# Kernel tuning notes

Measured on AMD Instinct MI355X. Metric: run time of the kernel, lower is better.

The kernel has to match this reference:

```python
import jax, jax.numpy as jnp
import numpy as np

B, T, D, H = 16, 512, 512, 8
TE = 2048
DH = D // H


def _ln(x, g, b, eps=1e-5):
    m = jnp.mean(x, axis=-1, keepdims=True)
    v = jnp.mean((x - m) ** 2, axis=-1, keepdims=True)
    return (x - m) * jax.lax.rsqrt(v + eps) * g + b


def setup_inputs() -> dict:
    key = jax.random.key(0)
    ks = jax.random.split(key, 16)
    s = 0.02
    inp = {
        "x1": jax.random.normal(ks[0], (B, T, D), jnp.float32),
        "x2": jax.random.normal(ks[1], (B, T, D), jnp.float32),
        "emb": jax.random.normal(ks[2], (2 * B, TE), jnp.float32),
        "src_mask": jnp.ones((2 * B, T, T, 1), jnp.float32),
        # LayerNorm params (x-norm and text-norm)
        "ln_x_g": jnp.ones((D,), jnp.float32), "ln_x_b": jnp.zeros((D,), jnp.float32),
        "ln_t_g": jnp.ones((D,), jnp.float32), "ln_t_b": jnp.zeros((D,), jnp.float32),
        # Q/K/V projections, stored as [in, out]
        "Wq": jax.random.normal(ks[3], (D, D), jnp.float32) * s, "bq": jnp.zeros((D,), jnp.float32),
        "Wk": jax.random.normal(ks[4], (D, D), jnp.float32) * s, "bk": jnp.zeros((D,), jnp.float32),
        "Wv": jax.random.normal(ks[5], (D, D), jnp.float32) * s, "bv": jnp.zeros((D,), jnp.float32),
        # StylizationBlock: SiLU->Linear(TE, 2D), LayerNorm(D), SiLU->Linear(D, D)
        "Wemb": jax.random.normal(ks[6], (TE, 2 * D), jnp.float32) * s, "bemb": jnp.zeros((2 * D,), jnp.float32),
        "sb_g": jnp.ones((D,), jnp.float32), "sb_b": jnp.zeros((D,), jnp.float32),
        "Wout": jax.random.normal(ks[7], (D, D), jnp.float32) * s, "bout": jnp.zeros((D,), jnp.float32),
    }
    return inp


def reference(x1, x2, emb, src_mask,
              ln_x_g, ln_x_b, ln_t_g, ln_t_b,
              Wq, bq, Wk, bk, Wv, bv,
              Wemb, bemb, sb_g, sb_b, Wout, bout):
    # cross=True: swap-concat the two interacting streams
    xa = jnp.concatenate([x1, x2], axis=0)  # [2B,T,D] (query side)
    xb = jnp.concatenate([x2, x1], axis=0)  # [2B,T,D] (key/value side)
    B2 = xa.shape[0]

    xn = _ln(xa, ln_x_g, ln_x_b)
    tn = _ln(xb, ln_t_g, ln_t_b)

    q = (xn @ Wq + bq).reshape(B2, T, H, DH)
    k = (tn @ Wk + bk).reshape(B2, T, H, DH)
    v = (tn @ Wv + bv).reshape(B2, T, H, DH)

    attn = jnp.einsum('bnhd,bmhd->bnmh', q, k) / np.sqrt(DH).astype(np.float32)
    attn = attn + (1.0 - src_mask) * -100000.0
    w = jax.nn.softmax(attn, axis=2)  # softmax over key axis m

    y = jnp.einsum('bnmh,bmhd->bnhd', w, v).reshape(B2, T, D)

    # StylizationBlock: FiLM from emb, then SiLU + Linear
    emb_out = (jax.nn.silu(emb) @ Wemb + bemb)[:, None, :]  # [2B,1,2D]
    scale, shift = jnp.split(emb_out, 2, axis=2)
    h = _ln(y, sb_g, sb_b) * (1.0 + scale) + shift
    h = jax.nn.silu(h) @ Wout + bout

    out = xa + h
    return out[:B2 // 2], out[B2 // 2:]
```

## Files before the change

### kernel.cpp

```cpp
#include <hip/hip_runtime.h>
#include <hip/hip_bf16.h>
#include <stdint.h>


typedef float f32x4 __attribute__((ext_vector_type(4)));
typedef short s16x8 __attribute__((ext_vector_type(8)));

#define MFMA16(a, b, c) __builtin_amdgcn_mfma_f32_16x16x32_bf16((a), (b), (c), 0, 0, 0)
#define GLD16(g, l) __builtin_amdgcn_global_load_lds( \
    (const __attribute__((address_space(1))) void*)(g), \
    (__attribute__((address_space(3))) void*)(l), 16, 0, 0)

__device__ __forceinline__ ushort f2bf(float f) {
    union { float f; uint32_t u; } cv; cv.f = f;
    uint32_t u = cv.u;
    return (ushort)((u + 0x7fffu + ((u >> 16) & 1u)) >> 16);
}
__device__ __forceinline__ float bf2f(ushort u) {
    union { uint32_t u; float f; } cv; cv.u = ((uint32_t)u) << 16;
    return cv.f;
}
__device__ __forceinline__ uint32_t pack_bf2(float a, float b) {
    union { float f; uint32_t u; } x, y; x.f = a; y.f = b;
    return ((x.u + 0x8000u) >> 16) | ((y.u + 0x8000u) & 0xffff0000u);
}
__device__ __forceinline__ float fast_exp2(float x) {
#if __has_builtin(__builtin_amdgcn_exp2f)
    return __builtin_amdgcn_exp2f(x);
#else
    return exp2f(x);
#endif
}
__device__ __forceinline__ float wave_sum(float v) {
#pragma unroll
    for (int o = 32; o > 0; o >>= 1) v += __shfl_xor(v, o);
    return v;
}

#define QSCALE 0.180336880f
#define MNEG  -144269.504f

__global__ __launch_bounds__(256) void prep(
    const float* __restrict__ w0, const float* __restrict__ w1,
    const float* __restrict__ w2, const float* __restrict__ w3,
    ushort* __restrict__ o0, ushort* __restrict__ o1,
    ushort* __restrict__ o2, ushort* __restrict__ o3,
    const float* __restrict__ x1, const float* __restrict__ x2,
    const float* __restrict__ gx, const float* __restrict__ bx,
    const float* __restrict__ gt, const float* __restrict__ bt,
    ushort* __restrict__ xn, ushort* __restrict__ tn,
    const float* __restrict__ mask, int* __restrict__ flags,
    const float* __restrict__ bemb, float* __restrict__ ss) {
    __shared__ float tile[32][33];
    __shared__ int bad4[4];
    const int bid = blockIdx.x, tid = threadIdx.x;

    if (bid < 1024) {
        const int z = bid >> 8, xy = bid & 255;
        const float* src; ushort* dst;
        switch (z) {
            case 0: src = w0; dst = o0; break;
            case 1: src = w1; dst = o1; break;
            case 2: src = w2; dst = o2; break;
            default: src = w3; dst = o3; break;
        }
        const int n0 = (xy & 15) * 32, k0 = (xy >> 4) * 32;
        const int x = tid & 31, y0 = tid >> 5;
#pragma unroll
        for (int i = 0; i < 4; i++) {
            int yy = y0 + 8 * i;
            tile[yy][x] = src[(size_t)(k0 + yy) * 512 + n0 + x];
        }
        __syncthreads();
#pragma unroll
        for (int i = 0; i < 4; i++) {
            int yy = y0 + 8 * i;
            dst[(size_t)(n0 + yy) * 512 + k0 + x] = f2bf(tile[x][yy]);
        }
    } else if (bid < 5120) {
        const int r = (bid - 1024) * 4 + (tid >> 6);
        const int lane = tid & 63;
        const float* src = (r < 8192) ? x1 + (size_t)r * 512
                                      : x2 + (size_t)(r - 8192) * 512;
        const int tr = (r < 8192) ? r + 8192 : r - 8192;
        const int d0 = lane * 4;
        float4 a0 = *(const float4*)&src[d0];
        float4 a1 = *(const float4*)&src[d0 + 256];
        float s = a0.x + a0.y + a0.z + a0.w + a1.x + a1.y + a1.z + a1.w;
        float q = a0.x*a0.x + a0.y*a0.y + a0.z*a0.z + a0.w*a0.w
                + a1.x*a1.x + a1.y*a1.y + a1.z*a1.z + a1.w*a1.w;
        s = wave_sum(s); q = wave_sum(q);
        const float mean = s * (1.f/512.f);
        const float var = q * (1.f/512.f) - mean * mean;
        const float rs = rsqrtf(var + 1e-5f);
        float vals[8] = {a0.x, a0.y, a0.z, a0.w, a1.x, a1.y, a1.z, a1.w};
        ushort* px = xn + (size_t)r * 512;
        ushort* pt = tn + (size_t)tr * 512;
#pragma unroll
        for (int half = 0; half < 2; half++) {
            ushort4 ox, ot;
            ushort* pox = (ushort*)&ox; ushort* pot = (ushort*)&ot;
#pragma unroll
            for (int j = 0; j < 4; j++) {
                int d = d0 + half * 256 + j;
                float nv = (vals[half * 4 + j] - mean) * rs;
                pox[j] = f2bf(nv * gx[d] + bx[d]);
                pot[j] = f2bf(nv * gt[d] + bt[d]);
            }
            *(ushort4*)&px[d0 + half * 256] = ox;
            *(ushort4*)&pt[d0 + half * 256] = ot;
        }
    } else if (bid < 7168) {
        const int b = bid - 5120;
        const int b2 = b >> 6, qt = (b >> 3) & 7, kt = b & 7;
        const int r = tid >> 2, c4 = tid & 3;
        const float* mrow = mask + ((size_t)(b2 * 512 + qt * 64 + r)) * 512 + kt * 64;
        bool bad = false;
#pragma unroll
        for (int j = 0; j < 4; j++) {
            float4 v = *(const float4*)&mrow[(c4 + 4 * j) * 4];
            bad |= (v.x != 1.f) | (v.y != 1.f) | (v.z != 1.f) | (v.w != 1.f);
        }
        unsigned long long bl = __ballot(bad);
        const int w = tid >> 6;
        if ((tid & 63) == 0) bad4[w] = (bl != 0ull);
        __syncthreads();
        if (tid == 0) flags[b] = bad4[0] | bad4[1] | bad4[2] | bad4[3];
    } else {
        int i = (bid - 7168) * 256 + tid;
        ss[i] = bemb[i & 1023];
    }
}

__global__ __launch_bounds__(256) void emb_gemm(const float* __restrict__ emb,
                                                const float* __restrict__ Wemb,
                                                float* __restrict__ ss) {
    __shared__ float es[32 * 128];
    const int n0 = blockIdx.x * 128, k0 = blockIdx.y * 128;
    const int t = threadIdx.x;
#pragma unroll
    for (int i = 0; i < 16; i++) {
        int idx = t + 256 * i;
        int b = idx >> 7, kk = idx & 127;
        float v = emb[(size_t)b * 2048 + k0 + kk];
        es[idx] = v / (1.f + __expf(-v));
    }
    __syncthreads();
    const int n = n0 + (t & 127);
    const int kh = (t >> 7) * 64;
    float acc[32];
#pragma unroll
    for (int b = 0; b < 32; b++) acc[b] = 0.f;
    for (int kk = kh; kk < kh + 64; kk++) {
        float w = Wemb[(size_t)(k0 + kk) * 1024 + n];
#pragma unroll
        for (int b = 0; b < 32; b++) acc[b] += es[b * 128 + kk] * w;
    }
#pragma unroll
    for (int b = 0; b < 32; b++) atomicAdd(&ss[b * 1024 + n], acc[b]);
}

__global__ __launch_bounds__(256, 3) void gemm_qkv(
    const ushort* __restrict__ xn, const ushort* __restrict__ tn,
    const ushort* __restrict__ W,
    const float* __restrict__ bq, const float* __restrict__ bk,
    const float* __restrict__ bv,
    ushort* __restrict__ qb, ushort* __restrict__ kb,
    ushort* __restrict__ vtb) {
    __shared__ ushort As[128 * 64];
    __shared__ ushort Bs[128 * 64];
    const int tid = threadIdx.x;
    const int lane = tid & 63, w = tid >> 6;
    const int l15 = lane & 15, quad = lane >> 4;
    const int l8 = lane >> 3, c_src = (lane & 7) ^ l8;
    const int bid = blockIdx.x;
    const int xcd = bid & 7, j = bid >> 3;
    const int mt_l = j / 12, nt = j % 12;
    const int m0 = (xcd * 16 + mt_l) * 128, n0 = nt * 128;
    const ushort* A = (n0 < 512) ? xn : tn;
    const int wm = (w >> 1) * 64, wn = (w & 1) * 64;

    f32x4 zero = {0.f, 0.f, 0.f, 0.f};
    f32x4 acc[4][4];
#pragma unroll
    for (int i = 0; i < 4; i++)
#pragma unroll
        for (int jj = 0; jj < 4; jj++) acc[i][jj] = zero;

    const ushort* ga0 = A + (size_t)(m0 + w * 32 + l8) * 512 + c_src * 8;
    const ushort* gb0 = W + (size_t)(n0 + w * 32 + l8) * 512 + c_src * 8;

    for (int k0 = 0; k0 < 512; k0 += 64) {
#pragma unroll
        for (int i = 0; i < 4; i++) {
            GLD16(ga0 + (size_t)(i * 8) * 512 + k0, &As[(w * 32 + i * 8) * 64]);
            GLD16(gb0 + (size_t)(i * 8) * 512 + k0, &Bs[(w * 32 + i * 8) * 64]);
        }
        __syncthreads();
#pragma unroll
        for (int ks = 0; ks < 2; ks++) {
            const int sl = ((ks * 4 + quad) ^ (l15 & 7)) * 8;
            s16x8 af[4], bf[4];
#pragma unroll
            for (int i = 0; i < 4; i++)
                af[i] = *(const s16x8*)&As[(wm + i * 16 + l15) * 64 + sl];
#pragma unroll
            for (int jj = 0; jj < 4; jj++)
                bf[jj] = *(const s16x8*)&Bs[(wn + jj * 16 + l15) * 64 + sl];
#pragma unroll
            for (int i = 0; i < 4; i++)
#pragma unroll
                for (int jj = 0; jj < 4; jj++)
                    acc[i][jj] = MFMA16(af[i], bf[jj], acc[i][jj]);
        }
        __syncthreads();
    }

#pragma unroll
    for (int i = 0; i < 4; i++)
#pragma unroll
        for (int jj = 0; jj < 4; jj++) {
            const int col = n0 + wn + jj * 16 + l15;
            if (n0 < 512) {
                const float bvv = bq[col];
#pragma unroll
                for (int reg = 0; reg < 4; reg++) {
                    const int row = m0 + wm + i * 16 + quad * 4 + reg;
                    qb[(size_t)row * 512 + col] = f2bf((acc[i][jj][reg] + bvv) * QSCALE);
                }
            } else if (n0 < 1024) {
                const int ck = col - 512;
                const float bvv = bk[ck];
#pragma unroll
                for (int reg = 0; reg < 4; reg++) {
                    const int row = m0 + wm + i * 16 + quad * 4 + reg;
                    kb[(size_t)row * 512 + ck] = f2bf(acc[i][jj][reg] + bvv);
                }
            } else {
                const int c2 = col - 1024;
                const float bvv = bv[c2];
                const int b2 = m0 >> 9;
                const int t0 = (m0 & 511) + wm + i * 16 + quad * 4;
                ushort4 o4; ushort* po = (ushort*)&o4;
#pragma unroll
                for (int reg = 0; reg < 4; reg++)
                    po[reg] = f2bf(acc[i][jj][reg] + bvv);
                *(ushort4*)&vtb[((size_t)((b2 * 8 + (c2 >> 6)) * 64 + (c2 & 63))) * 512 + t0] = o4;
            }
        }
}

__global__ __launch_bounds__(256, 3) void gemm_out(
    const ushort* __restrict__ A, const ushort* __restrict__ Bt,
    const float* __restrict__ bias, float* __restrict__ of,
    const float* __restrict__ r1, const float* __restrict__ r2) {
    __shared__ ushort As[128 * 64];
    __shared__ ushort Bs[128 * 64];
    const int tid = threadIdx.x;
    const int lane = tid & 63, w = tid >> 6;
    const int l15 = lane & 15, quad = lane >> 4;
    const int l8 = lane >> 3, c_src = (lane & 7) ^ l8;
    const int bid = blockIdx.x;
    const int xcd = bid & 7, j2 = bid >> 3;
    const int m0 = (xcd * 16 + (j2 >> 2)) * 128;
    const int n0 = (j2 & 3) * 128;
    const int wm = (w >> 1) * 64, wn = (w & 1) * 64;

    f32x4 zero = {0.f, 0.f, 0.f, 0.f};
    f32x4 acc[4][4];
#pragma unroll
    for (int i = 0; i < 4; i++)
#pragma unroll
        for (int jj = 0; jj < 4; jj++) acc[i][jj] = zero;

    const ushort* ga0 = A + (size_t)(m0 + w * 32 + l8) * 512 + c_src * 8;
    const ushort* gb0 = Bt + (size_t)(n0 + w * 32 + l8) * 512 + c_src * 8;

    for (int k0 = 0; k0 < 512; k0 += 64) {
#pragma unroll
        for (int i = 0; i < 4; i++) {
            GLD16(ga0 + (size_t)(i * 8) * 512 + k0, &As[(w * 32 + i * 8) * 64]);
            GLD16(gb0 + (size_t)(i * 8) * 512 + k0, &Bs[(w * 32 + i * 8) * 64]);
        }
        __syncthreads();
#pragma unroll
        for (int ks = 0; ks < 2; ks++) {
            const int sl = ((ks * 4 + quad) ^ (l15 & 7)) * 8;
            s16x8 af[4], bf[4];
#pragma unroll
            for (int i = 0; i < 4; i++)
                af[i] = *(const s16x8*)&As[(wm + i * 16 + l15) * 64 + sl];
#pragma unroll
            for (int jj = 0; jj < 4; jj++)
                bf[jj] = *(const s16x8*)&Bs[(wn + jj * 16 + l15) * 64 + sl];
#pragma unroll
            for (int i = 0; i < 4; i++)
#pragma unroll
                for (int jj = 0; jj < 4; jj++)
                    acc[i][jj] = MFMA16(af[i], bf[jj], acc[i][jj]);
        }
        __syncthreads();
    }

#pragma unroll
    for (int i = 0; i < 4; i++)
#pragma unroll
        for (int jj = 0; jj < 4; jj++) {
            const int col = n0 + wn + jj * 16 + l15;
            const float bvv = bias[col];
#pragma unroll
            for (int reg = 0; reg < 4; reg++) {
                const int row = m0 + wm + i * 16 + quad * 4 + reg;
                float res = (row < 8192)
                                ? r1[(size_t)row * 512 + col]
                                : r2[(size_t)(row - 8192) * 512 + col];
                of[(size_t)row * 512 + col] = acc[i][jj][reg] + bvv + res;
            }
        }
}

__global__ __launch_bounds__(256) void attn(
    const ushort* __restrict__ q, const ushort* __restrict__ k,
    const ushort* __restrict__ vt, const float* __restrict__ mask,
    const int* __restrict__ flags, ushort* __restrict__ y) {
    __shared__ ushort Ks[2][64 * 64];
    __shared__ ushort Vs[2][64 * 64];
    __shared__ ushort Ps[4][16 * 72];
    const int tid = threadIdx.x;
    const int lane = tid & 63, w = tid >> 6;
    const int l15 = lane & 15, quad = lane >> 4;
    const int l8 = lane >> 3, c_src = (lane & 7) ^ l8;
    const int bh = blockIdx.x, qt = blockIdx.y;
    const int b2 = bh >> 3, h = bh & 7;
    const int qrow0 = qt * 64 + w * 16;

    s16x8 qf0, qf1;
    {
        const ushort* qp = q + ((size_t)(b2 * 512 + qrow0 + l15)) * 512 + h * 64 + quad * 8;
        qf0 = *(const s16x8*)qp;
        qf1 = *(const s16x8*)(qp + 32);
    }
    f32x4 zero = {0.f, 0.f, 0.f, 0.f};
    f32x4 o[4];
#pragma unroll
    for (int nt = 0; nt < 4; nt++) o[nt] = zero;
    float l_i = 0.f;

    const ushort* kg0 = k + ((size_t)(b2 * 512 + w * 16 + l8)) * 512 + h * 64 + c_src * 8;
    const ushort* vg0 = vt + ((size_t)(bh * 64 + w * 16 + l8)) * 512 + c_src * 8;
    ushort* Pw = &Ps[w][0];
    const int slq = (quad ^ (l15 & 7)) * 8;
    const int slq4 = ((4 + quad) ^ (l15 & 7)) * 8;
    const int fl_base = (b2 * 8 + qt) * 8;

    auto stage = [&](int buf, int kt) {
        GLD16(kg0 + (size_t)(kt * 64) * 512, &Ks[buf][(w * 16) * 64]);
        GLD16(kg0 + (size_t)(kt * 64 + 8) * 512, &Ks[buf][(w * 16 + 8) * 64]);
        GLD16(vg0 + kt * 64, &Vs[buf][(w * 16) * 64]);
        GLD16(vg0 + (size_t)8 * 512 + kt * 64, &Vs[buf][(w * 16 + 8) * 64]);
    };
    stage(0, 0);

    for (int kt = 0; kt < 8; kt++) {
        __syncthreads();
        if (kt < 7) stage((kt + 1) & 1, kt + 1);
        const ushort* Kb = Ks[kt & 1];
        const ushort* Vb = Vs[kt & 1];

        f32x4 st[4];
#pragma unroll
        for (int mt = 0; mt < 4; mt++) {
            const int row = (mt * 16 + l15) * 64;
            s16x8 kf0 = *(const s16x8*)&Kb[row + slq];
            s16x8 kf1 = *(const s16x8*)&Kb[row + slq4];
            st[mt] = MFMA16(kf0, qf0, zero);
            st[mt] = MFMA16(kf1, qf1, st[mt]);
        }

        if (flags[fl_base + kt]) {
            const size_t mb = ((size_t)(b2 * 512 + qt * 64 + w * 16 + l15)) * 512 + kt * 64;
#pragma unroll
            for (int mt = 0; mt < 4; mt++)
#pragma unroll
                for (int reg = 0; reg < 4; reg++)
                    st[mt][reg] += (1.f - mask[mb + mt * 16 + quad * 4 + reg]) * MNEG;
        }

        float psum = 0.f;
#pragma unroll
        for (int mt = 0; mt < 4; mt++) {
            float p0 = fast_exp2(st[mt][0]);
            float p1 = fast_exp2(st[mt][1]);
            float p2 = fast_exp2(st[mt][2]);
            float p3 = fast_exp2(st[mt][3]);
            psum += (p0 + p1) + (p2 + p3);
            uint2 pk;
            pk.x = pack_bf2(p0, p1);
            pk.y = pack_bf2(p2, p3);
            *(uint2*)&Pw[l15 * 72 + mt * 16 + quad * 4] = pk;
        }

        s16x8 pf0 = *(const s16x8*)&Pw[l15 * 72 + quad * 8];
        s16x8 pf1 = *(const s16x8*)&Pw[l15 * 72 + 32 + quad * 8];
#pragma unroll
        for (int nt = 0; nt < 4; nt++) {
            const int vr = (nt * 16 + l15) * 64;
            s16x8 vf0 = *(const s16x8*)&Vb[vr + slq];
            s16x8 vf1 = *(const s16x8*)&Vb[vr + slq4];
            o[nt] = MFMA16(pf0, vf0, o[nt]);
            o[nt] = MFMA16(pf1, vf1, o[nt]);
        }

        psum += __shfl_xor(psum, 16);
        psum += __shfl_xor(psum, 32);
        l_i += psum;
    }

    const float invl = 1.f / l_i;
    float ir[4];
#pragma unroll
    for (int reg = 0; reg < 4; reg++) ir[reg] = __shfl(invl, quad * 4 + reg);
#pragma unroll
    for (int reg = 0; reg < 4; reg++) {
        const int row = qt * 64 + w * 16 + quad * 4 + reg;
        ushort* yp = y + ((size_t)(b2 * 512 + row)) * 512 + h * 64;
#pragma unroll
        for (int nt = 0; nt < 4; nt++)
            yp[nt * 16 + l15] = f2bf(o[nt][reg] * ir[reg]);
    }
}

__global__ __launch_bounds__(256) void film_silu(
    const ushort* __restrict__ y, const float* __restrict__ g,
    const float* __restrict__ b, const float* __restrict__ ss,
    ushort* __restrict__ tb) {
    const int r = blockIdx.x * 4 + (threadIdx.x >> 6);
    const int lane = threadIdx.x & 63;
    const int b2 = r >> 9;
    const int d0 = lane * 8;
    s16x8 raw = *(const s16x8*)&y[(size_t)r * 512 + d0];
    float v[8];
#pragma unroll
    for (int j = 0; j < 8; j++) v[j] = bf2f((ushort)raw[j]);
    float s = 0.f, qq = 0.f;
#pragma unroll
    for (int j = 0; j < 8; j++) { s += v[j]; qq += v[j] * v[j]; }
    s = wave_sum(s); qq = wave_sum(qq);
    const float mean = s * (1.f/512.f);
    const float var = qq * (1.f/512.f) - mean * mean;
    const float rs = rsqrtf(var + 1e-5f);
    const float* scp = ss + (size_t)b2 * 1024;
    s16x8 o;
#pragma unroll
    for (int j = 0; j < 8; j++) {
        int d = d0 + j;
        float ln = (v[j] - mean) * rs * g[d] + b[d];
        float hv = ln * (1.f + scp[d]) + scp[512 + d];
        o[j] = (short)f2bf(hv / (1.f + __expf(-hv)));
    }
    *(s16x8*)&tb[(size_t)r * 512 + d0] = o;
}

extern "C" void kernel_launch(void* const* d_in, const int* in_sizes, int n_in,
                              void* d_out, int out_size, void* d_ws, size_t ws_size,
                              hipStream_t stream) {
    const float* x1     = (const float*)d_in[0];
    const float* x2     = (const float*)d_in[1];
    const float* emb    = (const float*)d_in[2];
    const float* mask   = (const float*)d_in[3];
    const float* ln_x_g = (const float*)d_in[4];
    const float* ln_x_b = (const float*)d_in[5];
    const float* ln_t_g = (const float*)d_in[6];
    const float* ln_t_b = (const float*)d_in[7];
    const float* Wq     = (const float*)d_in[8];
    const float* bq     = (const float*)d_in[9];
    const float* Wk     = (const float*)d_in[10];
    const float* bk     = (const float*)d_in[11];
    const float* Wv     = (const float*)d_in[12];
    const float* bv     = (const float*)d_in[13];
    const float* Wemb   = (const float*)d_in[14];
    const float* bemb   = (const float*)d_in[15];
    const float* sb_g   = (const float*)d_in[16];
    const float* sb_b   = (const float*)d_in[17];
    const float* Wout   = (const float*)d_in[18];
    const float* bout   = (const float*)d_in[19];
    float* out = (float*)d_out;

    char* ws = (char*)d_ws;
    ushort* xn   = (ushort*)(ws + 0);
    ushort* tn   = (ushort*)(ws + (16u << 20));
    ushort* qb   = (ushort*)(ws + (32u << 20));
    ushort* kb   = (ushort*)(ws + (48u << 20));
    ushort* vtb  = (ushort*)(ws + (64u << 20));
    ushort* yb   = (ushort*)(ws + (80u << 20));
    ushort* wqkv = (ushort*)(ws + (96u << 20));
    ushort* wto  = wqkv + 786432;
    float*  ss   = (float*)(ws + (98u << 20));
    int*    flg  = (int*)(ws + (98u << 20) + (128u << 10));
    ushort* tb   = xn;

    prep<<<7296, 256, 0, stream>>>(Wq, Wk, Wv, Wout,
                                   wqkv, wqkv + 262144, wqkv + 524288, wto,
                                   x1, x2, ln_x_g, ln_x_b, ln_t_g, ln_t_b, xn, tn,
                                   mask, flg, bemb, ss);

    emb_gemm<<<dim3(8, 16), 256, 0, stream>>>(emb, Wemb, ss);

    gemm_qkv<<<1536, 256, 0, stream>>>(xn, tn, wqkv, bq, bk, bv, qb, kb, vtb);

    attn<<<dim3(256, 8), 256, 0, stream>>>(qb, kb, vtb, mask, flg, yb);

    film_silu<<<4096, 256, 0, stream>>>(yb, sb_g, sb_b, ss, tb);

    gemm_out<<<512, 256, 0, stream>>>(tb, wto, bout, out, x1, x2);

    (void)in_sizes; (void)n_in; (void)out_size; (void)ws_size;
}
```

Baseline: 294.3 us.

## Load K/V attention fragments directly from global into registers, dropping LDS staging

The attention kernel no longer stages K and V tiles in shared memory with async global-to-LDS copies and per-tile barriers. Each wave now loads its K and V MFMA fragments straight from global memory into registers and prefetches the next K tile one iteration ahead. It also sets a launch bound of three blocks per CU. This removes the __syncthreads and LDS traffic, but each of the four waves now fetches the same K/V data separately and register pressure rises, which may force spills.

```diff
diff --git a/kernel.cpp b/kernel.cpp
--- a/kernel.cpp
+++ b/kernel.cpp
@@ -319,17 +319,14 @@
         }
 }
 
-__global__ __launch_bounds__(256) void attn(
+__global__ __launch_bounds__(256, 3) void attn(
     const ushort* __restrict__ q, const ushort* __restrict__ k,
     const ushort* __restrict__ vt, const float* __restrict__ mask,
     const int* __restrict__ flags, ushort* __restrict__ y) {
-    __shared__ ushort Ks[2][64 * 64];
-    __shared__ ushort Vs[2][64 * 64];
     __shared__ ushort Ps[4][16 * 72];
     const int tid = threadIdx.x;
     const int lane = tid & 63, w = tid >> 6;
     const int l15 = lane & 15, quad = lane >> 4;
-    const int l8 = lane >> 3, c_src = (lane & 7) ^ l8;
     const int bh = blockIdx.x, qt = blockIdx.y;
     const int b2 = bh >> 3, h = bh & 7;
     const int qrow0 = qt * 64 + w * 16;
@@ -346,35 +343,42 @@
     for (int nt = 0; nt < 4; nt++) o[nt] = zero;
     float l_i = 0.f;
 
-    const ushort* kg0 = k + ((size_t)(b2 * 512 + w * 16 + l8)) * 512 + h * 64 + c_src * 8;
-    const ushort* vg0 = vt + ((size_t)(bh * 64 + w * 16 + l8)) * 512 + c_src * 8;
+    const ushort* kbase = k + ((size_t)(b2 * 512 + l15)) * 512 + h * 64 + quad * 8;
+    const ushort* vbase = vt + ((size_t)(bh * 64 + l15)) * 512 + quad * 8;
     ushort* Pw = &Ps[w][0];
-    const int slq = (quad ^ (l15 & 7)) * 8;
-    const int slq4 = ((4 + quad) ^ (l15 & 7)) * 8;
     const int fl_base = (b2 * 8 + qt) * 8;
 
-    auto stage = [&](int buf, int kt) {
-        GLD16(kg0 + (size_t)(kt * 64) * 512, &Ks[buf][(w * 16) * 64]);
-        GLD16(kg0 + (size_t)(kt * 64 + 8) * 512, &Ks[buf][(w * 16 + 8) * 64]);
-        GLD16(vg0 + kt * 64, &Vs[buf][(w * 16) * 64]);
-        GLD16(vg0 + (size_t)8 * 512 + kt * 64, &Vs[buf][(w * 16 + 8) * 64]);
-    };
-    stage(0, 0);
+    s16x8 kc[8];
+#pragma unroll
+    for (int mt = 0; mt < 4; mt++) {
+        const ushort* p = kbase + (size_t)(mt * 16) * 512;
+        kc[2 * mt] = *(const s16x8*)p;
+        kc[2 * mt + 1] = *(const s16x8*)(p + 32);
+    }
 
     for (int kt = 0; kt < 8; kt++) {
-        __syncthreads();
-        if (kt < 7) stage((kt + 1) & 1, kt + 1);
-        const ushort* Kb = Ks[kt & 1];
-        const ushort* Vb = Vs[kt & 1];
+        s16x8 vf[8];
+#pragma unroll
+        for (int nt = 0; nt < 4; nt++) {
+            const ushort* p = vbase + (size_t)(nt * 16) * 512 + kt * 64;
+            vf[2 * nt] = *(const s16x8*)p;
+            vf[2 * nt + 1] = *(const s16x8*)(p + 32);
+        }
+        s16x8 kn[8];
+        if (kt < 7) {
+#pragma unroll
+            for (int mt = 0; mt < 4; mt++) {
+                const ushort* p = kbase + (size_t)((kt + 1) * 64 + mt * 16) * 512;
+                kn[2 * mt] = *(const s16x8*)p;
+                kn[2 * mt + 1] = *(const s16x8*)(p + 32);
+            }
+        }
 
         f32x4 st[4];
 #pragma unroll
         for (int mt = 0; mt < 4; mt++) {
-            const int row = (mt * 16 + l15) * 64;
-            s16x8 kf0 = *(const s16x8*)&Kb[row + slq];
-            s16x8 kf1 = *(const s16x8*)&Kb[row + slq4];
-            st[mt] = MFMA16(kf0, qf0, zero);
-            st[mt] = MFMA16(kf1, qf1, st[mt]);
+            st[mt] = MFMA16(kc[2 * mt], qf0, zero);
+            st[mt] = MFMA16(kc[2 * mt + 1], qf1, st[mt]);
         }
 
         if (flags[fl_base + kt]) {
@@ -404,16 +408,16 @@
         s16x8 pf1 = *(const s16x8*)&Pw[l15 * 72 + 32 + quad * 8];
 #pragma unroll
         for (int nt = 0; nt < 4; nt++) {
-            const int vr = (nt * 16 + l15) * 64;
-            s16x8 vf0 = *(const s16x8*)&Vb[vr + slq];
-            s16x8 vf1 = *(const s16x8*)&Vb[vr + slq4];
-            o[nt] = MFMA16(pf0, vf0, o[nt]);
-            o[nt] = MFMA16(pf1, vf1, o[nt]);
+            o[nt] = MFMA16(pf0, vf[2 * nt], o[nt]);
+            o[nt] = MFMA16(pf1, vf[2 * nt + 1], o[nt]);
         }
 
         psum += __shfl_xor(psum, 16);
         psum += __shfl_xor(psum, 32);
         l_i += psum;
+
+#pragma unroll
+        for (int i = 0; i < 8; i++) kc[i] = kn[i];
     }
 
     const float invl = 1.f / l_i;
```

After: 373.0 us. 26.7% more time.

## Process 32 query rows per wave in attention to reuse K/V tiles

Applied to the files above, without the earlier changes.

Each attention wave now handles two 16-row query sub-tiles instead of one, so every K and V fragment read from LDS feeds twice as many MFMAs. The grid's query-tile dimension is halved, which halves total K/V global-to-LDS staging. Mask flag indexing is adjusted to the 64-row flag granularity, and launch bounds request 3 blocks per CU. The cost is more registers per thread for the doubled accumulators, a larger P buffer in LDS, and fewer blocks in the grid.

```diff
diff --git a/kernel.cpp b/kernel.cpp
--- a/kernel.cpp
+++ b/kernel.cpp
@@ -319,39 +319,42 @@
         }
 }
 
-__global__ __launch_bounds__(256) void attn(
+__global__ __launch_bounds__(256, 3) void attn(
     const ushort* __restrict__ q, const ushort* __restrict__ k,
     const ushort* __restrict__ vt, const float* __restrict__ mask,
     const int* __restrict__ flags, ushort* __restrict__ y) {
     __shared__ ushort Ks[2][64 * 64];
     __shared__ ushort Vs[2][64 * 64];
-    __shared__ ushort Ps[4][16 * 72];
+    __shared__ ushort Ps[4][32 * 72];
     const int tid = threadIdx.x;
     const int lane = tid & 63, w = tid >> 6;
     const int l15 = lane & 15, quad = lane >> 4;
     const int l8 = lane >> 3, c_src = (lane & 7) ^ l8;
     const int bh = blockIdx.x, qt = blockIdx.y;
     const int b2 = bh >> 3, h = bh & 7;
-    const int qrow0 = qt * 64 + w * 16;
-
-    s16x8 qf0, qf1;
-    {
-        const ushort* qp = q + ((size_t)(b2 * 512 + qrow0 + l15)) * 512 + h * 64 + quad * 8;
-        qf0 = *(const s16x8*)qp;
-        qf1 = *(const s16x8*)(qp + 32);
+    const int qrow0 = qt * 128 + w * 32;
+
+    s16x8 qf[2][2];
+#pragma unroll
+    for (int qi = 0; qi < 2; qi++) {
+        const ushort* qp = q + ((size_t)(b2 * 512 + qrow0 + qi * 16 + l15)) * 512 + h * 64 + quad * 8;
+        qf[qi][0] = *(const s16x8*)qp;
+        qf[qi][1] = *(const s16x8*)(qp + 32);
     }
     f32x4 zero = {0.f, 0.f, 0.f, 0.f};
-    f32x4 o[4];
-#pragma unroll
-    for (int nt = 0; nt < 4; nt++) o[nt] = zero;
-    float l_i = 0.f;
+    f32x4 o[2][4];
+#pragma unroll
+    for (int qi = 0; qi < 2; qi++)
+#pragma unroll
+        for (int nt = 0; nt < 4; nt++) o[qi][nt] = zero;
+    float l_i[2] = {0.f, 0.f};
 
     const ushort* kg0 = k + ((size_t)(b2 * 512 + w * 16 + l8)) * 512 + h * 64 + c_src * 8;
     const ushort* vg0 = vt + ((size_t)(bh * 64 + w * 16 + l8)) * 512 + c_src * 8;
     ushort* Pw = &Ps[w][0];
     const int slq = (quad ^ (l15 & 7)) * 8;
     const int slq4 = ((4 + quad) ^ (l15 & 7)) * 8;
-    const int fl_base = (b2 * 8 + qt) * 8;
+    const int fl_base = (b2 * 8 + qt * 2 + (w >> 1)) * 8;
 
     auto stage = [&](int buf, int kt) {
         GLD16(kg0 + (size_t)(kt * 64) * 512, &Ks[buf][(w * 16) * 64]);
@@ -367,66 +370,82 @@
         const ushort* Kb = Ks[kt & 1];
         const ushort* Vb = Vs[kt & 1];
 
-        f32x4 st[4];
+        f32x4 st[2][4];
 #pragma unroll
         for (int mt = 0; mt < 4; mt++) {
             const int row = (mt * 16 + l15) * 64;
             s16x8 kf0 = *(const s16x8*)&Kb[row + slq];
             s16x8 kf1 = *(const s16x8*)&Kb[row + slq4];
-            st[mt] = MFMA16(kf0, qf0, zero);
-            st[mt] = MFMA16(kf1, qf1, st[mt]);
+            st[0][mt] = MFMA16(kf0, qf[0][0], zero);
+            st[0][mt] = MFMA16(kf1, qf[0][1], st[0][mt]);
+            st[1][mt] = MFMA16(kf0, qf[1][0], zero);
+            st[1][mt] = MFMA16(kf1, qf[1][1], st[1][mt]);
         }
 
         if (flags[fl_base + kt]) {
-            const size_t mb = ((size_t)(b2 * 512 + qt * 64 + w * 16 + l15)) * 512 + kt * 64;
-#pragma unroll
-            for (int mt = 0; mt < 4; mt++)
-#pragma unroll
-                for (int reg = 0; reg < 4; reg++)
-                    st[mt][reg] += (1.f - mask[mb + mt * 16 + quad * 4 + reg]) * MNEG;
-        }
-
-        float psum = 0.f;
-#pragma unroll
-        for (int mt = 0; mt < 4; mt++) {
-            float p0 = fast_exp2(st[mt][0]);
-            float p1 = fast_exp2(st[mt][1]);
-            float p2 = fast_exp2(st[mt][2]);
-            float p3 = fast_exp2(st[mt][3]);
-            psum += (p0 + p1) + (p2 + p3);
-            uint2 pk;
-            pk.x = pack_bf2(p0, p1);
-            pk.y = pack_bf2(p2, p3);
-            *(uint2*)&Pw[l15 * 72 + mt * 16 + quad * 4] = pk;
-        }
-
-        s16x8 pf0 = *(const s16x8*)&Pw[l15 * 72 + quad * 8];
-        s16x8 pf1 = *(const s16x8*)&Pw[l15 * 72 + 32 + quad * 8];
+#pragma unroll
+            for (int qi = 0; qi < 2; qi++) {
+                const size_t mb = ((size_t)(b2 * 512 + qt * 128 + w * 32 + qi * 16 + l15)) * 512 + kt * 64;
+#pragma unroll
+                for (int mt = 0; mt < 4; mt++)
+#pragma unroll
+                    for (int reg = 0; reg < 4; reg++)
+                        st[qi][mt][reg] += (1.f - mask[mb + mt * 16 + quad * 4 + reg]) * MNEG;
+            }
+        }
+
+#pragma unroll
+        for (int qi = 0; qi < 2; qi++) {
+            float psum = 0.f;
+#pragma unroll
+            for (int mt = 0; mt < 4; mt++) {
+                float p0 = fast_exp2(st[qi][mt][0]);
+                float p1 = fast_exp2(st[qi][mt][1]);
+                float p2 = fast_exp2(st[qi][mt][2]);
+                float p3 = fast_exp2(st[qi][mt][3]);
+                psum += (p0 + p1) + (p2 + p3);
+                uint2 pk;
+                pk.x = pack_bf2(p0, p1);
+                pk.y = pack_bf2(p2, p3);
+                *(uint2*)&Pw[(qi * 16 + l15) * 72 + mt * 16 + quad * 4] = pk;
+            }
+            psum += __shfl_xor(psum, 16);
+            psum += __shfl_xor(psum, 32);
+            l_i[qi] += psum;
+        }
+
+        s16x8 pf[2][2];
+#pragma unroll
+        for (int qi = 0; qi < 2; qi++) {
+            pf[qi][0] = *(const s16x8*)&Pw[(qi * 16 + l15) * 72 + quad * 8];
+            pf[qi][1] = *(const s16x8*)&Pw[(qi * 16 + l15) * 72 + 32 + quad * 8];
+        }
 #pragma unroll
         for (int nt = 0; nt < 4; nt++) {
             const int vr = (nt * 16 + l15) * 64;
             s16x8 vf0 = *(const s16x8*)&Vb[vr + slq];
             s16x8 vf1 = *(const s16x8*)&Vb[vr + slq4];
-            o[nt] = MFMA16(pf0, vf0, o[nt]);
-            o[nt] = MFMA16(pf1, vf1, o[nt]);
-        }
-
-        psum += __shfl_xor(psum, 16);
-        psum += __shfl_xor(psum, 32);
-        l_i += psum;
-    }
-
-    const float invl = 1.f / l_i;
-    float ir[4];
-#pragma unroll
-    for (int reg = 0; reg < 4; reg++) ir[reg] = __shfl(invl, quad * 4 + reg);
-#pragma unroll
-    for (int reg = 0; reg < 4; reg++) {
-        const int row = qt * 64 + w * 16 + quad * 4 + reg;
-        ushort* yp = y + ((size_t)(b2 * 512 + row)) * 512 + h * 64;
-#pragma unroll
-        for (int nt = 0; nt < 4; nt++)
-            yp[nt * 16 + l15] = f2bf(o[nt][reg] * ir[reg]);
+            o[0][nt] = MFMA16(pf[0][0], vf0, o[0][nt]);
+            o[0][nt] = MFMA16(pf[0][1], vf1, o[0][nt]);
+            o[1][nt] = MFMA16(pf[1][0], vf0, o[1][nt]);
+            o[1][nt] = MFMA16(pf[1][1], vf1, o[1][nt]);
+        }
+    }
+
+#pragma unroll
+    for (int qi = 0; qi < 2; qi++) {
+        const float invl = 1.f / l_i[qi];
+        float ir[4];
+#pragma unroll
+        for (int reg = 0; reg < 4; reg++) ir[reg] = __shfl(invl, quad * 4 + reg);
+#pragma unroll
+        for (int reg = 0; reg < 4; reg++) {
+            const int row = qt * 128 + w * 32 + qi * 16 + quad * 4 + reg;
+            ushort* yp = y + ((size_t)(b2 * 512 + row)) * 512 + h * 64;
+#pragma unroll
+            for (int nt = 0; nt < 4; nt++)
+                yp[nt * 16 + l15] = f2bf(o[qi][nt][reg] * ir[reg]);
+        }
     }
 }
 
@@ -508,7 +527,7 @@
 
     gemm_qkv<<<1536, 256, 0, stream>>>(xn, tn, wqkv, bq, bk, bv, qb, kb, vtb);
 
-    attn<<<dim3(256, 8), 256, 0, stream>>>(qb, kb, vtb, mask, flg, yb);
+    attn<<<dim3(256, 4), 256, 0, stream>>>(qb, kb, vtb, mask, flg, yb);
 
     film_silu<<<4096, 256, 0, stream>>>(yb, sb_g, sb_b, ss, tb);
 
```

Measured after the change: 289.9 us. About the same (-1.5%).
